# Kernel tuning notes

Hardware: AMD Instinct MI355X
Metric: run time of the kernel (lower is better)

## Reference

```python
import jax, jax.numpy as jnp
import numpy as np

H = 2048      # hidden_dim
DI = 4096     # intermediate_size
N = 128       # state_size
NH = 64       # num_heads
P = 64        # head_dim
K = 4         # conv kernel
CH = 256      # chunk size
L = 4096      # seq len
DT_MIN, DT_MAX = 1e-3, 1e2


def setup_inputs() -> dict:
    key = jax.random.key(0)
    ks = jax.random.split(key, 8)
    conv_dim = DI + 2 * N
    x = jax.random.normal(ks[0], (L, H), jnp.float32)
    W_in = jax.random.normal(ks[1], (DI + 2 * N + NH, H), jnp.float32) / np.sqrt(H)
    conv_w = jax.random.normal(ks[2], (conv_dim, 1, K), jnp.float32) / np.sqrt(K)
    conv_b = jax.random.normal(ks[3], (conv_dim,), jnp.float32) * 0.01
    u = jax.random.uniform(ks[4], (NH,))
    dt = jnp.exp(u * (np.log(0.1) - np.log(0.001)) + np.log(0.001))
    dt = jnp.maximum(dt, 1e-4)
    dt_bias = dt + jnp.log(-jnp.expm1(-dt))   # inverse-softplus init
    A_log = jnp.log(jax.random.uniform(ks[5], (NH,), minval=1.0, maxval=16.0))
    D = jnp.ones((NH,), jnp.float32)
    norm_w = jnp.ones((DI,), jnp.float32)
    W_out = jax.random.normal(ks[6], (H, DI), jnp.float32) / np.sqrt(DI)
    return dict(x=x, W_in=W_in, conv_w=conv_w, conv_b=conv_b, dt_bias=dt_bias,
                A_log=A_log, D=D, norm_w=norm_w, W_out=W_out)


def _causal_decay(a):
    # a: [..., T] per-step log-decays -> exp(segment sum) as lower-tri [..., T, T]
    T = a.shape[-1]
    strict = jnp.tril(jnp.ones((T, T), bool), -1)
    full = jnp.tril(jnp.ones((T, T), bool), 0)
    s = jnp.cumsum(jnp.where(strict, a[..., None], 0.0), axis=-2)
    return jnp.where(full, jnp.exp(s), 0.0)


def reference(x, W_in, conv_w, conv_b, dt_bias, A_log, D, norm_w, W_out):
    conv_dim = DI + 2 * N
    xBCdt = x @ W_in.T                                  # [L, DI+2N+NH]
    xBC, dt = xBCdt[:, :conv_dim], xBCdt[:, conv_dim:]
    # causal depthwise conv1d + SiLU
    z = jax.lax.conv_general_dilated(
        xBC.T[None], conv_w, (1,), [(K - 1, 0)],
        dimension_numbers=('NCH', 'OIH', 'NCH'),
        feature_group_count=conv_dim)[0] + conv_b[:, None]
    xBC = jax.nn.silu(z.T)                              # [L, conv_dim]
    x_ssm = xBC[:, :DI].reshape(L, NH, P)
    Bm = xBC[:, DI:DI + N]                              # [L, N] shared over heads
    Cm = xBC[:, DI + N:]                                # [L, N]
    dt = jnp.clip(jax.nn.softplus(dt + dt_bias), DT_MIN, DT_MAX)  # [L, NH]
    A = -jnp.exp(A_log.astype(jnp.float32))             # [NH]
    dA = dt * A                                         # [L, NH]
    xdt = x_ssm * dt[:, :, None]                        # [L, NH, P]
    nc = L // CH
    xc = xdt.reshape(nc, CH, NH, P)
    Bc = Bm.reshape(nc, CH, N)
    Cc = Cm.reshape(nc, CH, N)
    dAc = dA.reshape(nc, CH, NH)
    A_cs = jnp.cumsum(dAc, axis=1)                      # [c, k, h]
    # intra-chunk (diagonal blocks)
    Lmat = _causal_decay(dAc.transpose(0, 2, 1))        # [c, h, k, k]
    Y_diag = jnp.einsum('ckn,csn,chks,cshp->ckhp', Cc, Bc, Lmat, xc)
    # per-chunk right states
    decay_states = jnp.exp(A_cs[:, -1:, :] - A_cs)      # [c, k, h]
    states = jnp.einsum('ckn,ckh,ckhp->chpn', Bc, decay_states, xc)
    # inter-chunk recurrence (no initial state)
    chunk_sum = A_cs[:, -1, :].T                        # [h, c]
    dec = _causal_decay(jnp.pad(chunk_sum, ((0, 0), (1, 0))))  # [h, c+1, c+1]
    states = jnp.concatenate([jnp.zeros((1, NH, P, N), states.dtype), states], 0)
    new_states = jnp.einsum('hzc,chpn->zhpn', dec, states)      # [c+1, h, p, n]
    prev = new_states[:-1]                              # [c, h, p, n]
    Y_off = jnp.einsum('ckn,chpn,ckh->ckhp', Cc, prev, jnp.exp(A_cs))
    Y = (Y_diag + Y_off).reshape(L, NH, P) + x_ssm * D[None, :, None]
    y = Y.reshape(L, DI)
    # RMSNorm
    var = jnp.mean(jnp.square(y.astype(jnp.float32)), -1, keepdims=True)
    y = (y * jax.lax.rsqrt(var + 1e-6)) * norm_w
    return y @ W_out.T
```

## Files before the change

### kernel.cpp

```cpp
#include <hip/hip_runtime.h>


typedef __bf16 bf16;
typedef __bf16 bf16x8 __attribute__((ext_vector_type(8)));
typedef __bf16 bf16x4 __attribute__((ext_vector_type(4)));
typedef float  f32x4  __attribute__((ext_vector_type(4)));

#define DEV static __device__ __forceinline__

DEV f32x4 mfma16(bf16x8 a, bf16x8 b, f32x4 c) {
  return __builtin_amdgcn_mfma_f32_16x16x32_bf16(a, b, c, 0, 0, 0);
}

DEV void gll16(const bf16* g, bf16* l) {
  __builtin_amdgcn_global_load_lds(
      (const __attribute__((address_space(1))) unsigned int*)g,
      (__attribute__((address_space(3))) unsigned int*)l, 16, 0, 0);
}

#define BAR()   asm volatile("s_barrier" ::: "memory")
#define VMW(n)  asm volatile("s_waitcnt vmcnt(" #n ")" ::: "memory")

template <int NT, int LD, bool DTC>
__global__ __launch_bounds__(256, 2) void gemm_kernel(
    const bf16* __restrict__ Abase, const bf16* __restrict__ Bbase,
    bf16* __restrict__ C0, bf16* __restrict__ C1, float* __restrict__ dtf,
    int ldc, int ntN) {
  __shared__ __align__(16) bf16 lds[3 * 12288];
  const int tid = threadIdx.x;
  const int wid = tid >> 6, lane = tid & 63;
  const int lrow = lane & 15;
  const int lc = lane >> 4;
  const int wm = wid & 1, wn = wid >> 1;
  const int bx = blockIdx.x / ntN, by = blockIdx.x % ntN;
  const int row0 = bx * 256, col0 = by * 128;
  const bf16* A = Abase + (size_t)blockIdx.y * (NT * 32);
  const bf16* B = Bbase + (size_t)blockIdx.y * (NT * 32);

  const bf16* gA[4];
  const bf16* gB[2];
#pragma unroll
  for (int q = 0; q < 4; ++q) {
    int P = q * 4096 + tid * 16;
    int Lq = P ^ (((P >> 7) & 3) << 4);
    int srow = Lq >> 6;
    int selem = (Lq & 63) >> 1;
    gA[q] = A + (size_t)(row0 + srow) * LD + selem;
  }
#pragma unroll
  for (int q = 0; q < 2; ++q) {
    int P = q * 4096 + tid * 16;
    int Lq = P ^ (((P >> 7) & 3) << 4);
    int srow = Lq >> 6;
    int selem = (Lq & 63) >> 1;
    gB[q] = B + (size_t)(col0 + srow) * LD + selem;
  }
  auto stage = [&](int s, int ko) {
    bf16* sl = lds + s * 12288;
#pragma unroll
    for (int q = 0; q < 4; ++q) gll16(gA[q] + ko, sl + q * 2048 + tid * 8);
#pragma unroll
    for (int q = 0; q < 2; ++q) gll16(gB[q] + ko, sl + 8192 + q * 2048 + tid * 8);
  };
  auto rdA = [&](int s, int m) -> bf16x8 {
    int row = wm * 128 + m * 16 + lrow;
    int off = row * 64 + ((lc ^ ((row >> 1) & 3)) << 4);
    return *(const bf16x8*)((const char*)lds + s * 24576 + off);
  };
  auto rdB = [&](int s, int n) -> bf16x8 {
    int row = wn * 64 + n * 16 + lrow;
    int off = row * 64 + ((lc ^ ((row >> 1) & 3)) << 4);
    return *(const bf16x8*)((const char*)lds + s * 24576 + 16384 + off);
  };

  f32x4 acc[8][4] = {};
  stage(0, 0);
  stage(1, 32);
  int rs = 0, ws = 2;
  for (int t = 0; t < NT; ++t) {
    if (t + 1 < NT) { VMW(6); } else { VMW(0); }
    BAR();
    if (t + 2 < NT) stage(ws, (t + 2) * 32);
    bf16x8 b0 = rdB(rs, 0), b1 = rdB(rs, 1), b2 = rdB(rs, 2), b3 = rdB(rs, 3);
#pragma unroll
    for (int m = 0; m < 8; ++m) {
      bf16x8 a = rdA(rs, m);
      acc[m][0] = mfma16(a, b0, acc[m][0]);
      acc[m][1] = mfma16(a, b1, acc[m][1]);
      acc[m][2] = mfma16(a, b2, acc[m][2]);
      acc[m][3] = mfma16(a, b3, acc[m][3]);
    }
    rs = (rs == 2) ? 0 : rs + 1;
    ws = (ws == 2) ? 0 : ws + 1;
  }
  bf16* C = blockIdx.y ? C1 : C0;
  const int orow = lc * 4;
#pragma unroll
  for (int m = 0; m < 8; ++m)
#pragma unroll
    for (int n = 0; n < 4; ++n)
#pragma unroll
      for (int i = 0; i < 4; ++i) {
        int r = row0 + wm * 128 + m * 16 + orow + i;
        int c = col0 + wn * 64 + n * 16 + lrow;
        C[(size_t)r * ldc + c] = (bf16)acc[m][n][i];
      }
  if (DTC && by == 34 && wn == 0) {
#pragma unroll
    for (int m = 0; m < 8; ++m)
#pragma unroll
      for (int n = 0; n < 4; ++n)
#pragma unroll
        for (int i = 0; i < 4; ++i) {
          int r = row0 + wm * 128 + m * 16 + orow + i;
          int h = n * 16 + lrow;
          dtf[(size_t)r * 64 + h] = acc[m][n][i];
        }
  }
}

__global__ __launch_bounds__(256) void add2b_kernel(
    const bf16* __restrict__ a, const bf16* __restrict__ b,
    float* __restrict__ o, long n8) {
  long i = (long)blockIdx.x * blockDim.x + threadIdx.x;
  long stride = (long)gridDim.x * blockDim.x;
  for (; i < n8; i += stride) {
    bf16x8 va = ((const bf16x8*)a)[i];
    bf16x8 vb = ((const bf16x8*)b)[i];
    float4 o0, o1;
    o0.x = (float)va[0] + (float)vb[0];
    o0.y = (float)va[1] + (float)vb[1];
    o0.z = (float)va[2] + (float)vb[2];
    o0.w = (float)va[3] + (float)vb[3];
    o1.x = (float)va[4] + (float)vb[4];
    o1.y = (float)va[5] + (float)vb[5];
    o1.z = (float)va[6] + (float)vb[6];
    o1.w = (float)va[7] + (float)vb[7];
    ((float4*)o)[i * 2] = o0;
    ((float4*)o)[i * 2 + 1] = o1;
  }
}

__global__ __launch_bounds__(256) void cast_f2b_kernel(
    const float* __restrict__ in, bf16* __restrict__ out, long n4) {
  long i = (long)blockIdx.x * blockDim.x + threadIdx.x;
  long stride = (long)gridDim.x * blockDim.x;
  for (; i < n4; i += stride) {
    float4 v = ((const float4*)in)[i];
    bf16x4 o = {(bf16)v.x, (bf16)v.y, (bf16)v.z, (bf16)v.w};
    ((bf16x4*)out)[i] = o;
  }
}

__global__ __launch_bounds__(256) void cast_pad_kernel(
    const float* __restrict__ in, bf16* __restrict__ out, long n4, long valid4) {
  long i = (long)blockIdx.x * blockDim.x + threadIdx.x;
  long stride = (long)gridDim.x * blockDim.x;
  for (; i < n4; i += stride) {
    bf16x4 o = {(bf16)0.f, (bf16)0.f, (bf16)0.f, (bf16)0.f};
    if (i < valid4) {
      float4 v = ((const float4*)in)[i];
      o = bf16x4{(bf16)v.x, (bf16)v.y, (bf16)v.z, (bf16)v.w};
    }
    ((bf16x4*)out)[i] = o;
  }
}

__global__ __launch_bounds__(256) void dt_scan_kernel(
    const float* __restrict__ dtf, const float* __restrict__ dt_bias,
    const float* __restrict__ A_log, float* __restrict__ dt,
    float* __restrict__ Acs, float* __restrict__ decayO,
    float* __restrict__ expAcs, float* __restrict__ csum) {
  const int c = blockIdx.x, h = blockIdx.y;
  const int k = threadIdx.x;
  const int t = c * 256 + k;
  __shared__ float buf[256];
  float raw = dtf[(size_t)t * 64 + h] + dt_bias[h];
  float dtv = raw > 20.f ? raw : log1pf(__expf(raw));
  dtv = fminf(fmaxf(dtv, 0.001f), 100.f);
  dt[(size_t)t * 64 + h] = dtv;
  float dA = -__expf(A_log[h]) * dtv;
  buf[k] = dA;
  __syncthreads();
  for (int off = 1; off < 256; off <<= 1) {
    float add = (k >= off) ? buf[k - off] : 0.f;
    __syncthreads();
    buf[k] += add;
    __syncthreads();
  }
  float v = buf[k];
  float total = buf[255];
  size_t base = (size_t)(c * 64 + h) * 256 + k;
  Acs[base] = v;
  expAcs[base] = __expf(v);
  decayO[base] = __expf(total - v);
  if (k == 0) csum[c * 64 + h] = total;
}

__global__ __launch_bounds__(256) void conv_kernel(
    const bf16* __restrict__ xbc, const float* __restrict__ conv_w,
    const float* __restrict__ conv_b, const float* __restrict__ dt,
    bf16* __restrict__ XS, bf16* __restrict__ XDT_T, bf16* __restrict__ Bm,
    bf16* __restrict__ BT, bf16* __restrict__ Cm) {
  const int t0 = blockIdx.x * 64;
  const int c0 = blockIdx.y * 64;
  __shared__ float lin[67 * 64];
  __shared__ bf16 tr[64 * 72];
  const int tid = threadIdx.x;
  for (int v = tid; v < 67 * 16; v += 256) {
    int r = v >> 4, c4 = (v & 15) * 4;
    int gt = t0 + r - 3;
    float4 f = {0.f, 0.f, 0.f, 0.f};
    if (gt >= 0) {
      bf16x4 b = *(const bf16x4*)(xbc + (size_t)gt * 4608 + c0 + c4);
      f.x = (float)b[0]; f.y = (float)b[1]; f.z = (float)b[2]; f.w = (float)b[3];
    }
    lin[r * 64 + c4 + 0] = f.x;
    lin[r * 64 + c4 + 1] = f.y;
    lin[r * 64 + c4 + 2] = f.z;
    lin[r * 64 + c4 + 3] = f.w;
  }
  __syncthreads();
  const int cl = tid & 63, tg = tid >> 6;
  const int ch = c0 + cl;
  const float w0 = conv_w[ch * 4 + 0], w1 = conv_w[ch * 4 + 1];
  const float w2 = conv_w[ch * 4 + 2], w3 = conv_w[ch * 4 + 3];
  const float bb = conv_b[ch];
  float vals[16];
  for (int j = 0; j < 16; ++j) {
    int tl = tg * 16 + j;
    float s = bb + lin[tl * 64 + cl] * w0 + lin[(tl + 1) * 64 + cl] * w1 +
              lin[(tl + 2) * 64 + cl] * w2 + lin[(tl + 3) * 64 + cl] * w3;
    vals[j] = s / (1.f + __expf(-s));
  }
  if (c0 < 4096) {
    const int hh = c0 >> 6;
    for (int j = 0; j < 16; ++j) {
      int t = t0 + tg * 16 + j;
      XS[(size_t)t * 4096 + ch] = (bf16)vals[j];
    }
    __syncthreads();
    for (int j = 0; j < 16; ++j) {
      int tl = tg * 16 + j;
      float dtv = dt[(size_t)(t0 + tl) * 64 + hh];
      tr[cl * 72 + tl] = (bf16)(vals[j] * dtv);
    }
    __syncthreads();
    int p = tid >> 2, toff = (tid & 3) * 16;
    bf16* dst = XDT_T + (size_t)(hh * 64 + p) * 4096 + t0 + toff;
    *(bf16x8*)(dst) = *(const bf16x8*)(tr + p * 72 + toff);
    *(bf16x8*)(dst + 8) = *(const bf16x8*)(tr + p * 72 + toff + 8);
  } else if (c0 < 4224) {
    const int n0 = c0 - 4096;
    for (int j = 0; j < 16; ++j) {
      int t = t0 + tg * 16 + j;
      Bm[(size_t)t * 128 + n0 + cl] = (bf16)vals[j];
    }
    __syncthreads();
    for (int j = 0; j < 16; ++j) tr[cl * 72 + tg * 16 + j] = (bf16)vals[j];
    __syncthreads();
    int p = tid >> 2, toff = (tid & 3) * 16;
    bf16* dst = BT + (size_t)(n0 + p) * 4096 + t0 + toff;
    *(bf16x8*)(dst) = *(const bf16x8*)(tr + p * 72 + toff);
    *(bf16x8*)(dst + 8) = *(const bf16x8*)(tr + p * 72 + toff + 8);
  } else {
    const int n0 = c0 - 4224;
    for (int j = 0; j < 16; ++j) {
      int t = t0 + tg * 16 + j;
      Cm[(size_t)t * 128 + n0 + cl] = (bf16)vals[j];
    }
  }
}

__global__ __launch_bounds__(256) void gmat_kernel(
    const bf16* __restrict__ Cm, const bf16* __restrict__ Bm,
    bf16* __restrict__ G) {
  const int c = blockIdx.x, kt = blockIdx.y, st = blockIdx.z;
  const int tid = threadIdx.x;
  const int wave = tid >> 6, lane = tid & 63;
  const int lrow = lane & 15, lk = (lane >> 4) * 8;
  const int wr = (wave >> 1) * 64, wc = (wave & 1) * 64;
  f32x4 acc[4][4] = {};
  for (int kk = 0; kk < 4; ++kk) {
    bf16x8 aF[4], bF[4];
    for (int m = 0; m < 4; ++m)
      aF[m] = *(const bf16x8*)(Cm + (size_t)(c * 256 + kt * 128 + wr + m * 16 + lrow) * 128 + kk * 32 + lk);
    for (int n = 0; n < 4; ++n)
      bF[n] = *(const bf16x8*)(Bm + (size_t)(c * 256 + st * 128 + wc + n * 16 + lrow) * 128 + kk * 32 + lk);
    for (int m = 0; m < 4; ++m)
      for (int n = 0; n < 4; ++n)
        acc[m][n] = mfma16(aF[m], bF[n], acc[m][n]);
  }
  const int orow = (lane >> 4) * 4;
  for (int m = 0; m < 4; ++m)
    for (int n = 0; n < 4; ++n)
      for (int i = 0; i < 4; ++i) {
        int k = kt * 128 + wr + m * 16 + orow + i;
        int s = st * 128 + wc + n * 16 + lrow;
        G[((size_t)c * 256 + k) * 256 + s] = (bf16)acc[m][n][i];
      }
}

__global__ __launch_bounds__(256) void states_kernel(
    const bf16* __restrict__ XDT_T, const bf16* __restrict__ BT,
    const float* __restrict__ decayO, float* __restrict__ states) {
  const int c = blockIdx.x, h = blockIdx.y;
  __shared__ bf16 Ap[64 * 264];
  __shared__ float sDec[256];
  const int tid = threadIdx.x;
  const int wave = tid >> 6, lane = tid & 63;
  const int lrow = lane & 15, lk = (lane >> 4) * 8;
  sDec[tid] = decayO[(size_t)(c * 64 + h) * 256 + tid];
  __syncthreads();
  {
    int p = tid >> 2, kb = (tid & 3) * 64;
    const bf16* src = XDT_T + (size_t)(h * 64 + p) * 4096 + c * 256 + kb;
    for (int j = 0; j < 8; ++j) {
      bf16x8 v = *(const bf16x8*)(src + j * 8);
      bf16x8 o;
      for (int i = 0; i < 8; ++i) o[i] = (bf16)((float)v[i] * sDec[kb + j * 8 + i]);
      *(bf16x8*)(Ap + p * 264 + kb + j * 8) = o;
    }
  }
  __syncthreads();
  const int nb = wave * 32;
  f32x4 acc[4][2] = {};
  for (int kk = 0; kk < 8; ++kk) {
    bf16x8 aF[4], bF[2];
    for (int m = 0; m < 4; ++m)
      aF[m] = *(const bf16x8*)(Ap + (m * 16 + lrow) * 264 + kk * 32 + lk);
    for (int n = 0; n < 2; ++n)
      bF[n] = *(const bf16x8*)(BT + (size_t)(nb + n * 16 + lrow) * 4096 + c * 256 + kk * 32 + lk);
    for (int m = 0; m < 4; ++m)
      for (int n = 0; n < 2; ++n)
        acc[m][n] = mfma16(aF[m], bF[n], acc[m][n]);
  }
  float* st = states + (size_t)(c * 64 + h) * 64 * 128;
  const int orow = (lane >> 4) * 4;
  for (int m = 0; m < 4; ++m)
    for (int n = 0; n < 2; ++n)
      for (int i = 0; i < 4; ++i)
        st[(size_t)(m * 16 + orow + i) * 128 + nb + n * 16 + lrow] = acc[m][n][i];
}

__global__ __launch_bounds__(128) void chunk_rec_kernel(
    const float* __restrict__ states, const float* __restrict__ csum,
    bf16* __restrict__ prev) {
  const int h = blockIdx.x, p = blockIdx.y;
  const int n = threadIdx.x;
  size_t base = (size_t)h * 64 * 128 + (size_t)p * 128 + n;
  float run = 0.f;
  for (int c = 0; c < 16; ++c) {
    size_t idx = (size_t)c * 64 * 64 * 128 + base;
    prev[idx] = (bf16)run;
    run = run * __expf(csum[c * 64 + h]) + states[idx];
  }
}

__global__ __launch_bounds__(256) void ydiag_kernel(
    const bf16* __restrict__ Cm, const bf16* __restrict__ prev,
    const bf16* __restrict__ Gb, const float* __restrict__ Acs,
    const float* __restrict__ expAcs, const bf16* __restrict__ XDT_T,
    bf16* __restrict__ Yb) {
  const int c = blockIdx.x, h = blockIdx.y;
  __shared__ float sAcs[256];
  __shared__ float sExp[256];
  __shared__ __align__(16) bf16 pv[64 * 136];
  __shared__ __align__(16) bf16 xd[64 * 264];
  const int tid = threadIdx.x;
  const int wave = tid >> 6, lane = tid & 63;
  const int lrow = lane & 15, lk = (lane >> 4) * 8;
  const int wv16 = wave * 16;
  sAcs[tid] = Acs[(size_t)(c * 64 + h) * 256 + tid];
  sExp[tid] = expAcs[(size_t)(c * 64 + h) * 256 + tid];
  {
    int r = tid >> 2, q = (tid & 3) * 32;
    const bf16* src = prev + (size_t)(c * 64 + h) * 8192 + r * 128 + q;
    bf16* dst = pv + r * 136 + q;
    for (int j = 0; j < 4; ++j)
      *(bf16x8*)(dst + j * 8) = *(const bf16x8*)(src + j * 8);
  }
  {
    int r = tid >> 2, q = (tid & 3) * 64;
    const bf16* src = XDT_T + (size_t)(h * 64 + r) * 4096 + c * 256 + q;
    bf16* dst = xd + r * 264 + q;
    for (int j = 0; j < 8; ++j)
      *(bf16x8*)(dst + j * 8) = *(const bf16x8*)(src + j * 8);
  }
  __syncthreads();
  f32x4 acc[4][4] = {};
  bf16x8 aYo[4][4];
#pragma unroll
  for (int kk = 0; kk < 4; ++kk)
#pragma unroll
    for (int m = 0; m < 4; ++m)
      aYo[kk][m] = *(const bf16x8*)(Cm + (size_t)(c * 256 + m * 64 + wv16 + lrow) * 128 + kk * 32 + lk);
#pragma unroll
  for (int kk = 0; kk < 4; ++kk) {
    bf16x8 bF[4];
#pragma unroll
    for (int n = 0; n < 4; ++n)
      bF[n] = *(const bf16x8*)(pv + (n * 16 + lrow) * 136 + kk * 32 + lk);
#pragma unroll
    for (int m = 0; m < 4; ++m)
#pragma unroll
      for (int n = 0; n < 4; ++n)
        acc[m][n] = mfma16(aYo[kk][m], bF[n], acc[m][n]);
  }
  const int orow = (lane >> 4) * 4;
#pragma unroll
  for (int m = 0; m < 4; ++m)
#pragma unroll
    for (int i = 0; i < 4; ++i) {
      float e = sExp[m * 64 + wv16 + orow + i];
      for (int n = 0; n < 4; ++n) acc[m][n][i] *= e;
    }
  const bf16* Gp = Gb + (size_t)c * 65536;
#pragma unroll
  for (int stile = 0; stile < 4; ++stile) {
    const int s0 = stile * 64;
    bf16x8 graw[2][4];
#pragma unroll
    for (int kk = 0; kk < 2; ++kk)
#pragma unroll
      for (int m = 0; m < 4; ++m)
        if (m * 64 + wv16 + 15 >= s0) {
          int row = m * 64 + wv16 + lrow;
          graw[kk][m] = *(const bf16x8*)(Gp + (size_t)row * 256 + s0 + kk * 32 + lk);
        }
    bf16x8 bF[2][4];
#pragma unroll
    for (int kk = 0; kk < 2; ++kk)
#pragma unroll
      for (int n = 0; n < 4; ++n)
        bF[kk][n] = *(const bf16x8*)(xd + (n * 16 + lrow) * 264 + s0 + kk * 32 + lk);
#pragma unroll
    for (int kk = 0; kk < 2; ++kk)
#pragma unroll
      for (int m = 0; m < 4; ++m) {
        if (m * 64 + wv16 + 15 < s0) continue;
        const int row = m * 64 + wv16 + lrow;
        const float ak = sAcs[row];
        bf16x8 af;
#pragma unroll
        for (int j = 0; j < 8; ++j) {
          int s = s0 + kk * 32 + lk + j;
          float v = (float)graw[kk][m][j] * __expf(ak - sAcs[s]);
          if (s > row) v = 0.f;
          af[j] = (bf16)v;
        }
#pragma unroll
        for (int n = 0; n < 4; ++n)
          acc[m][n] = mfma16(af, bF[kk][n], acc[m][n]);
      }
  }
#pragma unroll
  for (int m = 0; m < 4; ++m)
#pragma unroll
    for (int n = 0; n < 4; ++n)
#pragma unroll
      for (int i = 0; i < 4; ++i) {
        int t = c * 256 + m * 64 + wv16 + orow + i;
        int col = h * 64 + n * 16 + lrow;
        Yb[(size_t)t * 4096 + col] = (bf16)acc[m][n][i];
      }
}

__global__ __launch_bounds__(256) void rmsnorm_kernel(
    const bf16* __restrict__ Yb, const bf16* __restrict__ XS,
    const float* __restrict__ Dp, const float* __restrict__ norm_w,
    bf16* __restrict__ out) {
  const int row = blockIdx.x;
  const bf16x4* y4 = (const bf16x4*)(Yb + (size_t)row * 4096);
  const bf16x4* xs4 = (const bf16x4*)(XS + (size_t)row * 4096);
  float4 v[4];
  float ss = 0.f;
  for (int j = 0; j < 4; ++j) {
    int c4 = threadIdx.x + j * 256;
    bf16x4 yb = y4[c4];
    bf16x4 xs = xs4[c4];
    float d = Dp[(c4 * 4) >> 6];
    float4 y;
    y.x = (float)yb[0] + (float)xs[0] * d;
    y.y = (float)yb[1] + (float)xs[1] * d;
    y.z = (float)yb[2] + (float)xs[2] * d;
    y.w = (float)yb[3] + (float)xs[3] * d;
    v[j] = y;
    ss += y.x * y.x + y.y * y.y + y.z * y.z + y.w * y.w;
  }
  for (int off = 32; off; off >>= 1) ss += __shfl_down(ss, off, 64);
  __shared__ float ws[4];
  if ((threadIdx.x & 63) == 0) ws[threadIdx.x >> 6] = ss;
  __syncthreads();
  float scale = rsqrtf((ws[0] + ws[1] + ws[2] + ws[3]) / 4096.f + 1e-6f);
  for (int j = 0; j < 4; ++j) {
    int col = (threadIdx.x + j * 256) * 4;
    float4 w = *(const float4*)(norm_w + col);
    bf16x4 o = {(bf16)(v[j].x * scale * w.x), (bf16)(v[j].y * scale * w.y),
                (bf16)(v[j].z * scale * w.z), (bf16)(v[j].w * scale * w.w)};
    *(bf16x4*)(out + (size_t)row * 4096 + col) = o;
  }
}

extern "C" void kernel_launch(void* const* d_in, const int* in_sizes, int n_in,
                              void* d_out, int out_size, void* d_ws, size_t ws_size,
                              hipStream_t stream) {
  const float* x       = (const float*)d_in[0];
  const float* W_in    = (const float*)d_in[1];
  const float* conv_w  = (const float*)d_in[2];
  const float* conv_b  = (const float*)d_in[3];
  const float* dt_bias = (const float*)d_in[4];
  const float* A_log   = (const float*)d_in[5];
  const float* Dp      = (const float*)d_in[6];
  const float* norm_w  = (const float*)d_in[7];
  const float* W_out   = (const float*)d_in[8];

  size_t o = 0;
  char* base = (char*)d_ws;
  auto take = [&](size_t b) {
    char* p = base + o;
    o += (b + 255) & ~(size_t)255;
    return (void*)p;
  };
  bf16*  xb     = (bf16*)take((size_t)4096 * 2048 * 2);
  bf16*  winb   = (bf16*)take((size_t)4608 * 2048 * 2);
  bf16*  xbc    = (bf16*)take((size_t)4096 * 4608 * 2);
  float* dtf    = (float*)take((size_t)4096 * 64 * 4);
  float* dtg    = (float*)take((size_t)4096 * 64 * 4);
  float* Acs    = (float*)take((size_t)4096 * 64 * 4);
  float* decayO = (float*)take((size_t)4096 * 64 * 4);
  float* expA   = (float*)take((size_t)4096 * 64 * 4);
  float* csum   = (float*)take((size_t)16 * 64 * 4);
  bf16*  XS     = (bf16*)take((size_t)4096 * 4096 * 2);
  bf16*  XDT_T  = (bf16*)take((size_t)4096 * 4096 * 2);
  bf16*  Bm     = (bf16*)take((size_t)4096 * 128 * 2);
  bf16*  BT     = (bf16*)take((size_t)4096 * 128 * 2);
  bf16*  Cm     = (bf16*)take((size_t)4096 * 128 * 2);
  bf16*  Yb     = (bf16*)take((size_t)4096 * 4096 * 2);
  bf16*  prev   = (bf16*)take((size_t)16 * 64 * 64 * 128 * 2);
  bf16*  woutb  = (bf16*)take((size_t)2048 * 4096 * 2);
  bf16*  Gb     = (bf16*)((char*)xbc);
  float* states = (float*)((char*)xbc + (size_t)4194304);
  bf16*  ynorm  = xb;
  bf16*  p2a    = XS;
  bf16*  p2b    = XDT_T;

  cast_f2b_kernel<<<2048, 256, 0, stream>>>(x, xb, (long)4096 * 2048 / 4);
  cast_pad_kernel<<<2048, 256, 0, stream>>>(W_in, winb, (long)4608 * 2048 / 4,
                                            (long)4416 * 2048 / 4);
  gemm_kernel<64, 2048, true><<<dim3(576, 1), 256, 0, stream>>>(
      xb, winb, xbc, nullptr, dtf, 4608, 36);
  dt_scan_kernel<<<dim3(16, 64), 256, 0, stream>>>(dtf, dt_bias, A_log, dtg,
                                                   Acs, decayO, expA, csum);
  conv_kernel<<<dim3(64, 68), 256, 0, stream>>>(xbc, conv_w, conv_b, dtg, XS,
                                                XDT_T, Bm, BT, Cm);
  gmat_kernel<<<dim3(16, 2, 2), 256, 0, stream>>>(Cm, Bm, Gb);
  states_kernel<<<dim3(16, 64), 256, 0, stream>>>(XDT_T, BT, decayO, states);
  chunk_rec_kernel<<<dim3(64, 64), 128, 0, stream>>>(states, csum, prev);
  cast_f2b_kernel<<<2048, 256, 0, stream>>>(W_out, woutb, (long)2048 * 4096 / 4);
  ydiag_kernel<<<dim3(16, 64), 256, 0, stream>>>(Cm, prev, Gb, Acs, expA,
                                                 XDT_T, Yb);
  rmsnorm_kernel<<<4096, 256, 0, stream>>>(Yb, XS, Dp, norm_w, ynorm);
  gemm_kernel<64, 4096, false><<<dim3(256, 2), 256, 0, stream>>>(
      ynorm, woutb, p2a, p2b, nullptr, 2048, 16);
  add2b_kernel<<<2048, 256, 0, stream>>>(p2a, p2b, (float*)d_out,
                                         (long)4096 * 2048 / 8);
}
```

Before: 337.9 us.

## Use 8-wave GEMM blocks, merge cast kernels, store chunk states in bf16

The GEMM kernel now runs 512 threads (8 waves in a 4x2 grid) per 256x128 tile, so each wave holds a 64x64 accumulator instead of 128x64. This cuts register pressure and raises occupancy, and each thread issues fewer global-to-LDS loads per stage. The three fp32-to-bf16 cast launches are merged into one kernel, and the per-chunk states buffer is stored in bf16 rather than fp32 to halve its traffic. The bf16 states may lose precision in the inter-chunk recurrence, and each wave now reuses each B fragment across fewer MFMAs.

```diff
diff --git a/kernel.cpp b/kernel.cpp
--- a/kernel.cpp
+++ b/kernel.cpp
@@ -22,7 +22,7 @@
 #define VMW(n)  asm volatile("s_waitcnt vmcnt(" #n ")" ::: "memory")
 
 template <int NT, int LD, bool DTC>
-__global__ __launch_bounds__(256, 2) void gemm_kernel(
+__global__ __launch_bounds__(512, 4) void gemm_kernel(
     const bf16* __restrict__ Abase, const bf16* __restrict__ Bbase,
     bf16* __restrict__ C0, bf16* __restrict__ C1, float* __restrict__ dtf,
     int ldc, int ntN) {
@@ -31,39 +31,37 @@
   const int wid = tid >> 6, lane = tid & 63;
   const int lrow = lane & 15;
   const int lc = lane >> 4;
-  const int wm = wid & 1, wn = wid >> 1;
+  const int wm = wid & 3, wn = wid >> 2;
   const int bx = blockIdx.x / ntN, by = blockIdx.x % ntN;
   const int row0 = bx * 256, col0 = by * 128;
   const bf16* A = Abase + (size_t)blockIdx.y * (NT * 32);
   const bf16* B = Bbase + (size_t)blockIdx.y * (NT * 32);
 
-  const bf16* gA[4];
-  const bf16* gB[2];
-#pragma unroll
-  for (int q = 0; q < 4; ++q) {
-    int P = q * 4096 + tid * 16;
+  const bf16* gA[2];
+  const bf16* gB0;
+#pragma unroll
+  for (int q = 0; q < 2; ++q) {
+    int P = q * 8192 + tid * 16;
     int Lq = P ^ (((P >> 7) & 3) << 4);
     int srow = Lq >> 6;
     int selem = (Lq & 63) >> 1;
     gA[q] = A + (size_t)(row0 + srow) * LD + selem;
   }
-#pragma unroll
-  for (int q = 0; q < 2; ++q) {
-    int P = q * 4096 + tid * 16;
+  {
+    int P = tid * 16;
     int Lq = P ^ (((P >> 7) & 3) << 4);
     int srow = Lq >> 6;
     int selem = (Lq & 63) >> 1;
-    gB[q] = B + (size_t)(col0 + srow) * LD + selem;
+    gB0 = B + (size_t)(col0 + srow) * LD + selem;
   }
   auto stage = [&](int s, int ko) {
     bf16* sl = lds + s * 12288;
-#pragma unroll
-    for (int q = 0; q < 4; ++q) gll16(gA[q] + ko, sl + q * 2048 + tid * 8);
-#pragma unroll
-    for (int q = 0; q < 2; ++q) gll16(gB[q] + ko, sl + 8192 + q * 2048 + tid * 8);
+    gll16(gA[0] + ko, sl + tid * 8);
+    gll16(gA[1] + ko, sl + 4096 + tid * 8);
+    gll16(gB0 + ko, sl + 8192 + tid * 8);
   };
   auto rdA = [&](int s, int m) -> bf16x8 {
-    int row = wm * 128 + m * 16 + lrow;
+    int row = wm * 64 + m * 16 + lrow;
     int off = row * 64 + ((lc ^ ((row >> 1) & 3)) << 4);
     return *(const bf16x8*)((const char*)lds + s * 24576 + off);
   };
@@ -73,17 +71,17 @@
     return *(const bf16x8*)((const char*)lds + s * 24576 + 16384 + off);
   };
 
-  f32x4 acc[8][4] = {};
+  f32x4 acc[4][4] = {};
   stage(0, 0);
   stage(1, 32);
   int rs = 0, ws = 2;
   for (int t = 0; t < NT; ++t) {
-    if (t + 1 < NT) { VMW(6); } else { VMW(0); }
+    if (t + 1 < NT) { VMW(3); } else { VMW(0); }
     BAR();
     if (t + 2 < NT) stage(ws, (t + 2) * 32);
     bf16x8 b0 = rdB(rs, 0), b1 = rdB(rs, 1), b2 = rdB(rs, 2), b3 = rdB(rs, 3);
 #pragma unroll
-    for (int m = 0; m < 8; ++m) {
+    for (int m = 0; m < 4; ++m) {
       bf16x8 a = rdA(rs, m);
       acc[m][0] = mfma16(a, b0, acc[m][0]);
       acc[m][1] = mfma16(a, b1, acc[m][1]);
@@ -96,23 +94,23 @@
   bf16* C = blockIdx.y ? C1 : C0;
   const int orow = lc * 4;
 #pragma unroll
-  for (int m = 0; m < 8; ++m)
+  for (int m = 0; m < 4; ++m)
 #pragma unroll
     for (int n = 0; n < 4; ++n)
 #pragma unroll
       for (int i = 0; i < 4; ++i) {
-        int r = row0 + wm * 128 + m * 16 + orow + i;
+        int r = row0 + wm * 64 + m * 16 + orow + i;
         int c = col0 + wn * 64 + n * 16 + lrow;
         C[(size_t)r * ldc + c] = (bf16)acc[m][n][i];
       }
   if (DTC && by == 34 && wn == 0) {
 #pragma unroll
-    for (int m = 0; m < 8; ++m)
+    for (int m = 0; m < 4; ++m)
 #pragma unroll
       for (int n = 0; n < 4; ++n)
 #pragma unroll
         for (int i = 0; i < 4; ++i) {
-          int r = row0 + wm * 128 + m * 16 + orow + i;
+          int r = row0 + wm * 64 + m * 16 + orow + i;
           int h = n * 16 + lrow;
           dtf[(size_t)r * 64 + h] = acc[m][n][i];
         }
@@ -141,28 +139,31 @@
   }
 }
 
-__global__ __launch_bounds__(256) void cast_f2b_kernel(
-    const float* __restrict__ in, bf16* __restrict__ out, long n4) {
-  long i = (long)blockIdx.x * blockDim.x + threadIdx.x;
-  long stride = (long)gridDim.x * blockDim.x;
-  for (; i < n4; i += stride) {
-    float4 v = ((const float4*)in)[i];
-    bf16x4 o = {(bf16)v.x, (bf16)v.y, (bf16)v.z, (bf16)v.w};
-    ((bf16x4*)out)[i] = o;
-  }
-}
-
-__global__ __launch_bounds__(256) void cast_pad_kernel(
-    const float* __restrict__ in, bf16* __restrict__ out, long n4, long valid4) {
-  long i = (long)blockIdx.x * blockDim.x + threadIdx.x;
-  long stride = (long)gridDim.x * blockDim.x;
-  for (; i < n4; i += stride) {
+__global__ __launch_bounds__(256) void cast_all_kernel(
+    const float* __restrict__ x, bf16* __restrict__ xb,
+    const float* __restrict__ W_in, bf16* __restrict__ winb,
+    const float* __restrict__ W_out, bf16* __restrict__ woutb) {
+  const long stride = (long)gridDim.x * blockDim.x;
+  const long base = (long)blockIdx.x * blockDim.x + threadIdx.x;
+  const long nx = (long)4096 * 2048 / 4;
+  for (long i = base; i < nx; i += stride) {
+    float4 v = ((const float4*)x)[i];
+    ((bf16x4*)xb)[i] = bf16x4{(bf16)v.x, (bf16)v.y, (bf16)v.z, (bf16)v.w};
+  }
+  const long nw = (long)4608 * 2048 / 4;
+  const long nwv = (long)4416 * 2048 / 4;
+  for (long i = base; i < nw; i += stride) {
     bf16x4 o = {(bf16)0.f, (bf16)0.f, (bf16)0.f, (bf16)0.f};
-    if (i < valid4) {
-      float4 v = ((const float4*)in)[i];
+    if (i < nwv) {
+      float4 v = ((const float4*)W_in)[i];
       o = bf16x4{(bf16)v.x, (bf16)v.y, (bf16)v.z, (bf16)v.w};
     }
-    ((bf16x4*)out)[i] = o;
+    ((bf16x4*)winb)[i] = o;
+  }
+  const long no = (long)2048 * 4096 / 4;
+  for (long i = base; i < no; i += stride) {
+    float4 v = ((const float4*)W_out)[i];
+    ((bf16x4*)woutb)[i] = bf16x4{(bf16)v.x, (bf16)v.y, (bf16)v.z, (bf16)v.w};
   }
 }
 
@@ -303,7 +304,7 @@
 
 __global__ __launch_bounds__(256) void states_kernel(
     const bf16* __restrict__ XDT_T, const bf16* __restrict__ BT,
-    const float* __restrict__ decayO, float* __restrict__ states) {
+    const float* __restrict__ decayO, bf16* __restrict__ states) {
   const int c = blockIdx.x, h = blockIdx.y;
   __shared__ bf16 Ap[64 * 264];
   __shared__ float sDec[256];
@@ -335,16 +336,16 @@
       for (int n = 0; n < 2; ++n)
         acc[m][n] = mfma16(aF[m], bF[n], acc[m][n]);
   }
-  float* st = states + (size_t)(c * 64 + h) * 64 * 128;
+  bf16* st = states + (size_t)(c * 64 + h) * 64 * 128;
   const int orow = (lane >> 4) * 4;
   for (int m = 0; m < 4; ++m)
     for (int n = 0; n < 2; ++n)
       for (int i = 0; i < 4; ++i)
-        st[(size_t)(m * 16 + orow + i) * 128 + nb + n * 16 + lrow] = acc[m][n][i];
+        st[(size_t)(m * 16 + orow + i) * 128 + nb + n * 16 + lrow] = (bf16)acc[m][n][i];
 }
 
 __global__ __launch_bounds__(128) void chunk_rec_kernel(
-    const float* __restrict__ states, const float* __restrict__ csum,
+    const bf16* __restrict__ states, const float* __restrict__ csum,
     bf16* __restrict__ prev) {
   const int h = blockIdx.x, p = blockIdx.y;
   const int n = threadIdx.x;
@@ -353,7 +354,7 @@
   for (int c = 0; c < 16; ++c) {
     size_t idx = (size_t)c * 64 * 64 * 128 + base;
     prev[idx] = (bf16)run;
-    run = run * __expf(csum[c * 64 + h]) + states[idx];
+    run = run * __expf(csum[c * 64 + h]) + (float)states[idx];
   }
 }
 
@@ -540,16 +541,14 @@
   bf16*  prev   = (bf16*)take((size_t)16 * 64 * 64 * 128 * 2);
   bf16*  woutb  = (bf16*)take((size_t)2048 * 4096 * 2);
   bf16*  Gb     = (bf16*)((char*)xbc);
-  float* states = (float*)((char*)xbc + (size_t)4194304);
+  bf16*  states = (bf16*)((char*)xbc + (size_t)4194304);
   bf16*  ynorm  = xb;
   bf16*  p2a    = XS;
   bf16*  p2b    = XDT_T;
 
-  cast_f2b_kernel<<<2048, 256, 0, stream>>>(x, xb, (long)4096 * 2048 / 4);
-  cast_pad_kernel<<<2048, 256, 0, stream>>>(W_in, winb, (long)4608 * 2048 / 4,
-                                            (long)4416 * 2048 / 4);
-  gemm_kernel<64, 2048, true><<<dim3(576, 1), 256, 0, stream>>>(
-      xb, winb, xbc, nullptr, dtf, 4608, 36);
+  cast_all_kernel<<<2048, 256, 0, stream>>>(x, xb, W_in, winb, W_out, woutb);
+  gemm_kernel<64, 2048, true><<<dim3(576, 1), 512, 0, stream>>>(
+      xb, winb, xbc, xbc, dtf, 4608, 36);
   dt_scan_kernel<<<dim3(16, 64), 256, 0, stream>>>(dtf, dt_bias, A_log, dtg,
                                                    Acs, decayO, expA, csum);
   conv_kernel<<<dim3(64, 68), 256, 0, stream>>>(xbc, conv_w, conv_b, dtg, XS,
@@ -557,11 +556,10 @@
   gmat_kernel<<<dim3(16, 2, 2), 256, 0, stream>>>(Cm, Bm, Gb);
   states_kernel<<<dim3(16, 64), 256, 0, stream>>>(XDT_T, BT, decayO, states);
   chunk_rec_kernel<<<dim3(64, 64), 128, 0, stream>>>(states, csum, prev);
-  cast_f2b_kernel<<<2048, 256, 0, stream>>>(W_out, woutb, (long)2048 * 4096 / 4);
   ydiag_kernel<<<dim3(16, 64), 256, 0, stream>>>(Cm, prev, Gb, Acs, expA,
                                                  XDT_T, Yb);
   rmsnorm_kernel<<<4096, 256, 0, stream>>>(Yb, XS, Dp, norm_w, ynorm);
-  gemm_kernel<64, 4096, false><<<dim3(256, 2), 256, 0, stream>>>(
+  gemm_kernel<64, 4096, false><<<dim3(256, 2), 512, 0, stream>>>(
       ynorm, woutb, p2a, p2b, nullptr, 2048, 16);
   add2b_kernel<<<2048, 256, 0, stream>>>(p2a, p2b, (float*)d_out,
                                          (long)4096 * 2048 / 8);
```

Measured after the change: 327.8 us. 1.03x faster.
